# Performance work log

Measured on AMD Instinct MI355X. Metric: run time of the kernel, lower is better.

## Reference

```python
import jax, jax.numpy as jnp
import numpy as np

N_NODES = 32768
N_EDGES = 524288
NODE_DIM, POS_DIM, EDGE_DIM = 44, 8, 1
HID, OUT, LAYERS, HEADS = 128, 128, 3, 4
DK = HID // HEADS
LN_EPS = 1e-5


def _linear_w(key, fan_in, fan_out):
    return (jax.random.normal(key, (fan_in, fan_out), jnp.float32) / np.sqrt(fan_in)).astype(jnp.float32)


def _ln(x, g, b):
    m = jnp.mean(x, axis=-1, keepdims=True)
    v = jnp.var(x, axis=-1, keepdims=True)
    return (x - m) * jax.lax.rsqrt(v + LN_EPS) * g + b


def setup_inputs() -> dict:
    key = jax.random.key(0)
    ks = jax.random.split(key, 16)
    inp = {
        'feats': jax.random.normal(ks[0], (N_NODES, NODE_DIM), jnp.float32),
        'lap_pos_enc': jax.random.normal(ks[1], (N_NODES, POS_DIM), jnp.float32),
        'edge_feats': jax.random.normal(ks[2], (N_EDGES, EDGE_DIM), jnp.float32),
        'src': jax.random.randint(ks[3], (N_EDGES,), 0, N_NODES, jnp.int32),
        'dst': jax.random.randint(ks[4], (N_EDGES,), 0, N_NODES, jnp.int32),
        # input projections
        'W_node': _linear_w(ks[5], NODE_DIM, HID), 'b_node': jnp.zeros((HID,), jnp.float32),
        'W_pos': _linear_w(ks[6], POS_DIM, HID), 'b_pos': jnp.zeros((HID,), jnp.float32),
        'W_edge': _linear_w(ks[7], EDGE_DIM, HID), 'b_edge': jnp.zeros((HID,), jnp.float32),
    }
    # per-layer stacked params (all layers are HID->HID since OUT==HID)
    def stack(k, fi, fo):
        kk = jax.random.split(k, LAYERS)
        return jnp.stack([_linear_w(kk[i], fi, fo) for i in range(LAYERS)])
    inp['Wq'] = stack(ks[8], HID, HID)
    inp['Wk'] = stack(ks[9], HID, HID)
    inp['Wv'] = stack(ks[10], HID, HID)
    inp['We'] = stack(ks[11], HID, HID)
    inp['W_lin'] = stack(ks[12], HID, HID)
    inp['b_lin'] = jnp.zeros((LAYERS, HID), jnp.float32)
    inp['g1'] = jnp.ones((LAYERS, HID), jnp.float32)
    inp['be1'] = jnp.zeros((LAYERS, HID), jnp.float32)
    inp['Wf1'] = stack(ks[13], HID, 2 * HID)
    inp['bf1'] = jnp.zeros((LAYERS, 2 * HID), jnp.float32)
    inp['Wf2'] = stack(ks[14], 2 * HID, HID)
    inp['bf2'] = jnp.zeros((LAYERS, HID), jnp.float32)
    inp['g2'] = jnp.ones((LAYERS, HID), jnp.float32)
    inp['be2'] = jnp.zeros((LAYERS, HID), jnp.float32)
    return inp


def reference(feats, lap_pos_enc, edge_feats,
              W_node, b_node, W_pos, b_pos, W_edge, b_edge,
              Wq, Wk, Wv, We, W_lin, b_lin, g1, be1,
              Wf1, bf1, Wf2, bf2, g2, be2, src, dst):
    n = feats.shape[0]
    inv_sqrt_dk = np.float32(1.0 / np.sqrt(DK))
    h = feats @ W_node + b_node + lap_pos_enc @ W_pos + b_pos      # [N, HID]
    e = edge_feats @ W_edge + b_edge                               # [E, HID] (shared across layers)
    for i in range(LAYERS):
        Q = (h @ Wq[i]).reshape(n, HEADS, DK)
        K = (h @ Wk[i]).reshape(n, HEADS, DK)
        V = (h @ Wv[i]).reshape(n, HEADS, DK)
        E = (e @ We[i]).reshape(-1, HEADS, DK)                     # [E, H, DK]
        # raw score [E, H, 1] broadcast against (1+E) -> [E, H, DK] (faithful to source)
        score = jnp.sum(K[src] * Q[dst], axis=-1, keepdims=True) * inv_sqrt_dk
        score = score * (1.0 + E)
        alpha = jnp.exp(score)                                      # [E, H, DK]
        Z = jnp.maximum(jax.ops.segment_sum(alpha, dst, num_segments=n), 1e-6)
        h_out = jax.ops.segment_sum(V[src] * alpha, dst, num_segments=n) / Z
        h_out = h_out.reshape(n, HEADS * DK)
        h = h + h_out @ W_lin[i] + b_lin[i]                        # residual + dropout(identity)
        h = _ln(h, g1[i], be1[i])
        h2 = jax.nn.relu(h @ Wf1[i] + bf1[i]) @ Wf2[i] + bf2[i]
        h = _ln(h + h2, g2[i], be2[i])
    # dgl.mean_nodes over a single graph -> [1, OUT]; readout LayerNorm is never applied in source
    return jnp.mean(h, axis=0, keepdims=True)
```

## Files before the change

kernel.cpp:

```cpp
#include <hip/hip_runtime.h>
#include <hip/hip_bf16.h>

#define N_NODES 32768
#define N_EDGES 524288
#define LN_EPS 1e-5f

typedef unsigned short ushort_t;
typedef __attribute__((ext_vector_type(8))) short short8v;
typedef __attribute__((ext_vector_type(4))) float float4v;
typedef __attribute__((ext_vector_type(2))) float float2v;

__device__ __forceinline__ float bf2f(ushort_t u) {
    return __uint_as_float(((unsigned int)u) << 16);
}
__device__ __forceinline__ ushort_t f2bf(float f) {
    unsigned int u = __float_as_uint(f);
    unsigned int r = (u + 0x7FFFu + ((u >> 16) & 1u)) >> 16;
    return (ushort_t)r;
}
__device__ __forceinline__ float lo16(unsigned int x) { return __uint_as_float(x << 16); }
__device__ __forceinline__ float hi16(unsigned int x) { return __uint_as_float(x & 0xFFFF0000u); }

#if __has_builtin(__builtin_amdgcn_exp2f)
#define EXP2(x) __builtin_amdgcn_exp2f(x)
#else
#define EXP2(x) exp2f(x)
#endif

#define OFF_WNODE 0
#define OFF_BNODE 5632
#define OFF_WPOS  5760
#define OFF_BPOS  6784
#define OFF_WEDGE 6912
#define OFF_BEDGE 7040
#define OFF_BLIN  7168
#define OFF_G1    7552
#define OFF_BE1   7936
#define OFF_BF1   8320
#define OFF_BF2   9088
#define OFF_G2    9472
#define OFF_BE2   9856
#define CONV_TOTAL 10240

#define REC_QKV(i)  ((i) * 96)
#define REC_WLIN(i) (288 + (i) * 32)
#define REC_WF1(i)  (384 + (i) * 64)
#define REC_WF2(i)  (576 + (i) * 64)
#define REC_TOTAL   768

#define LDS_STRIDE 264
#define LDS_FSTRIDE 132

__global__ void detect_kernel(const unsigned int* __restrict__ wn, int* __restrict__ flag) {
    __shared__ int s[256];
    int t = threadIdx.x;
    int cnt = 0;
    for (int i = t; i < 2816; i += 256) {
        unsigned int b = (wn[i] >> 8) & 0x7F;
        cnt += (b >= 0x3A && b <= 0x40) ? 1 : 0;
    }
    s[t] = cnt;
    __syncthreads();
    for (int off = 128; off > 0; off >>= 1) {
        if (t < off) s[t] += s[t + off];
        __syncthreads();
    }
    if (t == 0) *flag = (s[0] > 1408) ? 1 : 0;
}

struct ConvArgs { const void* src[13]; };

__global__ void convert_kernel(ConvArgs a, const int* __restrict__ flag,
                               float* __restrict__ dst) {
    int gid = blockIdx.x * 256 + threadIdx.x;
    if (gid >= CONV_TOTAL) return;
    const int off[14] = {OFF_WNODE, OFF_BNODE, OFF_WPOS, OFF_BPOS, OFF_WEDGE, OFF_BEDGE,
                         OFF_BLIN, OFF_G1, OFF_BE1, OFF_BF1, OFF_BF2, OFF_G2, OFF_BE2,
                         CONV_TOTAL};
    int s = 0;
#pragma unroll
    for (int i = 1; i < 13; ++i) s += (gid >= off[i]) ? 1 : 0;
    int local = gid - off[s];
    if (*flag)
        dst[gid] = bf2f(((const ushort_t*)a.src[s])[local]);
    else
        dst[gid] = ((const float*)a.src[s])[local];
}

__global__ void swz_kernel(const void* __restrict__ Wq, const void* __restrict__ Wk,
                           const void* __restrict__ Wv, const void* __restrict__ Wlin,
                           const void* __restrict__ Wf1, const void* __restrict__ Wf2,
                           const void* __restrict__ We, const void* __restrict__ wedge,
                           const void* __restrict__ bedge,
                           const int* __restrict__ flag,
                           ushort_t* __restrict__ swz,
                           float* __restrict__ u, float* __restrict__ c1) {
    const bool isbf = (*flag != 0);
    if (blockIdx.x >= 192) {
        int l = blockIdx.x - 192;
        int d = threadIdx.x;
        if (d >= 128) return;
        float uu = 0.f, cc = 0.f;
        if (isbf) {
            const ushort_t* Wl = (const ushort_t*)We + (size_t)l * 16384;
            const ushort_t* we_ = (const ushort_t*)wedge;
            const ushort_t* be_ = (const ushort_t*)bedge;
#pragma unroll 4
            for (int k = 0; k < 128; ++k) {
                float w = bf2f(Wl[k * 128 + d]);
                uu = fmaf(bf2f(we_[k]), w, uu);
                cc = fmaf(bf2f(be_[k]), w, cc);
            }
        } else {
            const float* Wl = (const float*)We + (size_t)l * 16384;
            const float* we_ = (const float*)wedge;
            const float* be_ = (const float*)bedge;
#pragma unroll 4
            for (int k = 0; k < 128; ++k) {
                float w = Wl[k * 128 + d];
                uu = fmaf(we_[k], w, uu);
                cc = fmaf(be_[k], w, cc);
            }
        }
        const float scale = 0.17677669529663687f * 1.4426950408889634f;
        u[l * 128 + d] = uu * scale;
        c1[l * 128 + d] = (1.f + cc) * scale;
        return;
    }
    int gid = blockIdx.x * 256 + threadIdx.x;
    int lane = gid & 63;
    int rec = gid >> 6;
    int col = lane & 15, quad = lane >> 4;
    const void* src;
    size_t base;
    int ct, kb, OC;
    if (rec < 288) {
        int layer = rec / 96, r2 = rec % 96;
        ct = r2 >> 2; kb = r2 & 3;
        int seg = ct >> 3;
        src = (seg == 0) ? Wq : ((seg == 1) ? Wk : Wv);
        base = (size_t)layer * 16384; OC = 128; ct &= 7;
    } else if (rec < 384) {
        int r = rec - 288, layer = r / 32, r2 = r % 32;
        ct = r2 >> 2; kb = r2 & 3;
        src = Wlin; base = (size_t)layer * 16384; OC = 128;
    } else if (rec < 576) {
        int r = rec - 384, layer = r / 64, r2 = r % 64;
        ct = r2 >> 2; kb = r2 & 3;
        src = Wf1; base = (size_t)layer * 32768; OC = 256;
    } else {
        int r = rec - 576, layer = r / 64, r2 = r % 64;
        ct = r2 >> 3; kb = r2 & 7;
        src = Wf2; base = (size_t)layer * 32768; OC = 128;
    }
    int n = ct * 16 + col;
    ushort_t v[8];
    if (isbf) {
        const ushort_t* s16 = (const ushort_t*)src + base;
#pragma unroll
        for (int j = 0; j < 8; ++j) v[j] = s16[(size_t)(kb * 32 + quad * 8 + j) * OC + n];
    } else {
        const float* s32 = (const float*)src + base;
#pragma unroll
        for (int j = 0; j < 8; ++j) v[j] = f2bf(s32[(size_t)(kb * 32 + quad * 8 + j) * OC + n]);
    }
    ushort_t* o = swz + (size_t)rec * 512 + lane * 8;
#pragma unroll
    for (int j = 0; j < 8; ++j) o[j] = v[j];
}

__global__ void input_proj_kernel(const void* __restrict__ feats,
                                  const void* __restrict__ lap,
                                  const float* __restrict__ conv,
                                  const int* __restrict__ flag,
                                  const int* __restrict__ dstidx,
                                  int* __restrict__ deg,
                                  float* __restrict__ h, ushort_t* __restrict__ hb) {
    int gid = blockIdx.x * 256 + threadIdx.x;
    if (gid < N_EDGES) atomicAdd(&deg[dstidx[gid]], 1);
    int node = gid >> 5;
    int cg = (gid & 31) * 4;
    bool isbf = (*flag != 0);
    const float* Wn = conv + OFF_WNODE;
    const float* Wp = conv + OFF_WPOS;

    float4 b1 = *(const float4*)(conv + OFF_BNODE + cg);
    float4 b2 = *(const float4*)(conv + OFF_BPOS + cg);
    float a0 = b1.x + b2.x, a1 = b1.y + b2.y, a2 = b1.z + b2.z, a3 = b1.w + b2.w;

#define ACC(fv, Wbase, kk)                                            \
    {                                                                 \
        float4 wv_ = *(const float4*)(Wbase + (size_t)(kk) * 128 + cg); \
        a0 = fmaf(fv, wv_.x, a0);                                     \
        a1 = fmaf(fv, wv_.y, a1);                                     \
        a2 = fmaf(fv, wv_.z, a2);                                     \
        a3 = fmaf(fv, wv_.w, a3);                                     \
    }

    if (isbf) {
        const ushort_t* frow = (const ushort_t*)feats + (size_t)node * 44;
        const ushort_t* prow = (const ushort_t*)lap + (size_t)node * 8;
#pragma unroll
        for (int i = 0; i < 11; ++i) {
            ushort4 f = *(const ushort4*)(frow + i * 4);
            ACC(bf2f(f.x), Wn, i * 4 + 0)
            ACC(bf2f(f.y), Wn, i * 4 + 1)
            ACC(bf2f(f.z), Wn, i * 4 + 2)
            ACC(bf2f(f.w), Wn, i * 4 + 3)
        }
#pragma unroll
        for (int i = 0; i < 2; ++i) {
            ushort4 f = *(const ushort4*)(prow + i * 4);
            ACC(bf2f(f.x), Wp, i * 4 + 0)
            ACC(bf2f(f.y), Wp, i * 4 + 1)
            ACC(bf2f(f.z), Wp, i * 4 + 2)
            ACC(bf2f(f.w), Wp, i * 4 + 3)
        }
    } else {
        const float4* frow = (const float4*)((const float*)feats + (size_t)node * 44);
        const float4* prow = (const float4*)((const float*)lap + (size_t)node * 8);
#pragma unroll
        for (int i = 0; i < 11; ++i) {
            float4 f = frow[i];
            ACC(f.x, Wn, i * 4 + 0)
            ACC(f.y, Wn, i * 4 + 1)
            ACC(f.z, Wn, i * 4 + 2)
            ACC(f.w, Wn, i * 4 + 3)
        }
#pragma unroll
        for (int i = 0; i < 2; ++i) {
            float4 f = prow[i];
            ACC(f.x, Wp, i * 4 + 0)
            ACC(f.y, Wp, i * 4 + 1)
            ACC(f.z, Wp, i * 4 + 2)
            ACC(f.w, Wp, i * 4 + 3)
        }
    }
#undef ACC

    size_t idx = (size_t)node * 128 + cg;
    *(float4*)(h + idx) = make_float4(a0, a1, a2, a3);
    ushort4 ob;
    ob.x = f2bf(a0); ob.y = f2bf(a1); ob.z = f2bf(a2); ob.w = f2bf(a3);
    *(ushort4*)(hb + idx) = ob;
}

__global__ void scan_kernel(const int* __restrict__ deg, int* __restrict__ rowstart,
                            int* __restrict__ cursor) {
    __shared__ int lds[1024];
    int t = threadIdx.x;
    int base = t * 32;
    int v[32];
    int csum = 0;
#pragma unroll
    for (int j = 0; j < 8; ++j) {
        int4 x = *(const int4*)(deg + base + j * 4);
        v[j * 4 + 0] = x.x; v[j * 4 + 1] = x.y;
        v[j * 4 + 2] = x.z; v[j * 4 + 3] = x.w;
        csum += x.x + x.y + x.z + x.w;
    }
    lds[t] = csum;
    __syncthreads();
    for (int off = 1; off < 1024; off <<= 1) {
        int x = (t >= off) ? lds[t - off] : 0;
        __syncthreads();
        lds[t] += x;
        __syncthreads();
    }
    int excl = lds[t] - csum;
    int running = excl;
#pragma unroll
    for (int j = 0; j < 8; ++j) {
        int4 w;
        w.x = running; running += v[j * 4 + 0];
        w.y = running; running += v[j * 4 + 1];
        w.z = running; running += v[j * 4 + 2];
        w.w = running; running += v[j * 4 + 3];
        *(int4*)(rowstart + base + j * 4) = w;
        *(int4*)(cursor + base + j * 4) = w;
    }
    if (t == 1023) rowstart[N_NODES] = running;
}

__global__ void scatter_kernel(const int* __restrict__ src, const int* __restrict__ dst,
                               const void* __restrict__ ef, const int* __restrict__ flag,
                               int* __restrict__ cursor,
                               unsigned int* __restrict__ edges) {
    int e = blockIdx.x * 256 + threadIdx.x;
    if (e < N_EDGES) {
        ushort_t efb = (*flag != 0) ? ((const ushort_t*)ef)[e]
                                    : f2bf(((const float*)ef)[e]);
        int d = dst[e];
        int p = atomicAdd(&cursor[d], 1);
        edges[p] = (unsigned int)src[e] | ((unsigned int)efb << 16);
    }
}

template <int KB>
__global__ __launch_bounds__(256) void qkv_gemm(
    const ushort_t* __restrict__ A,
    const ushort_t* __restrict__ Bswz,
    ushort_t* __restrict__ outQ,
    unsigned char* __restrict__ outKV) {
    const int K = KB * 32;
    const int tid = threadIdx.x;
    const int wv = tid >> 6, lane = tid & 63;
    const int col = lane & 15, quad = lane >> 4;
    const int m0 = blockIdx.x * 64 + wv * 16;
    const int ct0 = blockIdx.y * 8;

    float4v acc[8];
#pragma unroll
    for (int ct = 0; ct < 8; ++ct) acc[ct] = (float4v){0.f, 0.f, 0.f, 0.f};

    const ushort_t* Ap = A + (size_t)(m0 + col) * K + quad * 8;
    const ushort_t* Bp = Bswz + (size_t)ct0 * KB * 512 + lane * 8;

#pragma unroll
    for (int kb = 0; kb < KB; ++kb) {
        short8v a = *(const short8v*)(Ap + kb * 32);
#pragma unroll
        for (int ct = 0; ct < 8; ++ct) {
            short8v b = *(const short8v*)(Bp + (size_t)(ct * KB + kb) * 512);
            acc[ct] = __builtin_amdgcn_mfma_f32_16x16x32_bf16(a, b, acc[ct], 0, 0, 0);
        }
    }

    const int rowb = m0 + quad * 4;
    const int seg = blockIdx.y;
    if (seg == 0) {
#pragma unroll
        for (int ct = 0; ct < 8; ++ct) {
            int j = ct * 16 + col;
#pragma unroll
            for (int r = 0; r < 4; ++r)
                outQ[(size_t)(rowb + r) * 128 + j] = f2bf(acc[ct][r]);
        }
    } else {
        const int vofs = (seg == 2) ? 8 : 0;
#pragma unroll
        for (int ct = 0; ct < 8; ++ct) {
            int j = ct * 16 + col;
            int off = ((j >> 3) * 16) + (j & 7) + vofs;
#pragma unroll
            for (int r = 0; r < 4; ++r) {
                float a = acc[ct][r];
                float b = __shfl_xor(a, 1, 64);
                if ((col & 1) == 0) {
                    unsigned short pk = (unsigned short)
                        __builtin_amdgcn_cvt_pk_fp8_f32(a, b, 0, false);
                    *(ushort_t*)(outKV + (size_t)(rowb + r) * 256 + off) = pk;
                }
            }
        }
    }
}

__global__ __launch_bounds__(64, 2) void ffn_kernel(
    const ushort_t* __restrict__ HOUT,
    const ushort_t* __restrict__ BWL,
    const ushort_t* __restrict__ BF1,
    const ushort_t* __restrict__ BF2,
    const ushort_t* __restrict__ BQKV,
    const float* __restrict__ bl,
    const float* __restrict__ g1v, const float* __restrict__ be1v,
    const float* __restrict__ bf1v,
    const float* __restrict__ bf2v,
    const float* __restrict__ g2v, const float* __restrict__ be2v,
    float* __restrict__ h,
    ushort_t* __restrict__ outQ,
    unsigned char* __restrict__ outKV,
    float* __restrict__ macc,
    const int fuse_qkv, const int do_mean) {
    __shared__ __align__(16) char ldsraw[16 * 528];
    ushort_t* ldsu = (ushort_t*)ldsraw;
    float* ldsf = (float*)ldsraw;
    const int lane = threadIdx.x & 63;
    const int col = lane & 15, quad = lane >> 4;
    const int m0 = blockIdx.x * 16;
    const int rowb = m0 + quad * 4;
    const int lrowc = quad * 4;
    const int lrowa = col;

    float4v acc[8];
#pragma unroll
    for (int ct = 0; ct < 8; ++ct) acc[ct] = (float4v){0.f, 0.f, 0.f, 0.f};
    const ushort_t* Ap = HOUT + (size_t)(m0 + col) * 128 + quad * 8;
#pragma unroll
    for (int kb = 0; kb < 4; ++kb) {
        short8v a = *(const short8v*)(Ap + kb * 32);
#pragma unroll
        for (int ct = 0; ct < 8; ++ct) {
            short8v b = *(const short8v*)(BWL + (size_t)(ct * 4 + kb) * 512 + lane * 8);
            acc[ct] = __builtin_amdgcn_mfma_f32_16x16x32_bf16(a, b, acc[ct], 0, 0, 0);
        }
    }

    float val[8][4], s[4] = {0.f, 0.f, 0.f, 0.f}, ss[4] = {0.f, 0.f, 0.f, 0.f};
#pragma unroll
    for (int ct = 0; ct < 8; ++ct) {
        float bi = bl[ct * 16 + col];
#pragma unroll
        for (int r = 0; r < 4; ++r) {
            float v = acc[ct][r] + bi + h[(size_t)(rowb + r) * 128 + ct * 16 + col];
            val[ct][r] = v;
            s[r] += v;
            ss[r] += v * v;
        }
    }
#pragma unroll
    for (int mask = 1; mask < 16; mask <<= 1) {
#pragma unroll
        for (int r = 0; r < 4; ++r) {
            s[r] += __shfl_xor(s[r], mask, 64);
            ss[r] += __shfl_xor(ss[r], mask, 64);
        }
    }
#pragma unroll
    for (int r = 0; r < 4; ++r) {
        float mean = s[r] * (1.f / 128.f);
        float var = ss[r] * (1.f / 128.f) - mean * mean;
        s[r] = mean;
        ss[r] = rsqrtf(var + LN_EPS);
    }
#pragma unroll
    for (int ct = 0; ct < 8; ++ct) {
        float gg = g1v[ct * 16 + col], bb = be1v[ct * 16 + col];
#pragma unroll
        for (int r = 0; r < 4; ++r) {
            float o = (val[ct][r] - s[r]) * ss[r] * gg + bb;
            val[ct][r] = o;
            ldsu[(lrowc + r) * LDS_STRIDE + ct * 16 + col] = f2bf(o);
        }
    }
    __syncthreads();

    short8v af[4];
#pragma unroll
    for (int kb = 0; kb < 4; ++kb)
        af[kb] = *(const short8v*)&ldsu[lrowa * LDS_STRIDE + kb * 32 + quad * 8];

    float4v acc2[16];
#pragma unroll
    for (int ct = 0; ct < 16; ++ct) acc2[ct] = (float4v){0.f, 0.f, 0.f, 0.f};
#pragma unroll
    for (int kb = 0; kb < 4; ++kb) {
#pragma unroll
        for (int ct = 0; ct < 16; ++ct) {
            short8v b = *(const short8v*)(BF1 + (size_t)(ct * 4 + kb) * 512 + lane * 8);
            acc2[ct] = __builtin_amdgcn_mfma_f32_16x16x32_bf16(af[kb], b, acc2[ct], 0, 0, 0);
        }
    }
    __syncthreads();

#pragma unroll
    for (int ct = 0; ct < 16; ++ct) {
        float bi = bf1v[ct * 16 + col];
#pragma unroll
        for (int r = 0; r < 4; ++r) {
            float v = fmaxf(acc2[ct][r] + bi, 0.f);
            ldsu[(lrowc + r) * LDS_STRIDE + ct * 16 + col] = f2bf(v);
        }
    }
    __syncthreads();

    float4v acc3[8];
#pragma unroll
    for (int ct = 0; ct < 8; ++ct) acc3[ct] = (float4v){0.f, 0.f, 0.f, 0.f};
#pragma unroll
    for (int kb = 0; kb < 8; ++kb) {
        short8v a = *(const short8v*)&ldsu[lrowa * LDS_STRIDE + kb * 32 + quad * 8];
#pragma unroll
        for (int ct = 0; ct < 8; ++ct) {
            short8v b = *(const short8v*)(BF2 + (size_t)(ct * 8 + kb) * 512 + lane * 8);
            acc3[ct] = __builtin_amdgcn_mfma_f32_16x16x32_bf16(a, b, acc3[ct], 0, 0, 0);
        }
    }

    float s2[4] = {0.f, 0.f, 0.f, 0.f}, ss2[4] = {0.f, 0.f, 0.f, 0.f};
#pragma unroll
    for (int ct = 0; ct < 8; ++ct) {
        float bi = bf2v[ct * 16 + col];
#pragma unroll
        for (int r = 0; r < 4; ++r) {
            float v = acc3[ct][r] + bi + val[ct][r];
            val[ct][r] = v;
            s2[r] += v;
            ss2[r] += v * v;
        }
    }
#pragma unroll
    for (int mask = 1; mask < 16; mask <<= 1) {
#pragma unroll
        for (int r = 0; r < 4; ++r) {
            s2[r] += __shfl_xor(s2[r], mask, 64);
            ss2[r] += __shfl_xor(ss2[r], mask, 64);
        }
    }
#pragma unroll
    for (int r = 0; r < 4; ++r) {
        float mean = s2[r] * (1.f / 128.f);
        float var = ss2[r] * (1.f / 128.f) - mean * mean;
        s2[r] = mean;
        ss2[r] = rsqrtf(var + LN_EPS);
    }
    __syncthreads();
#pragma unroll
    for (int ct = 0; ct < 8; ++ct) {
        float gg = g2v[ct * 16 + col], bb = be2v[ct * 16 + col];
#pragma unroll
        for (int r = 0; r < 4; ++r) {
            float o = (val[ct][r] - s2[r]) * ss2[r] * gg + bb;
            ldsf[(lrowc + r) * LDS_FSTRIDE + ct * 16 + col] = o;
        }
    }
    __syncthreads();

#pragma unroll
    for (int j = 0; j < 8; ++j) {
        int p = lane + j * 64;
        int row = p >> 5;
        int c4 = p & 31;
        float4 vv = *(const float4*)&ldsf[row * LDS_FSTRIDE + c4 * 4];
        *(float4*)&h[(size_t)(m0 + row) * 128 + c4 * 4] = vv;
    }

    if (fuse_qkv) {
        short8v afq[4];
#pragma unroll
        for (int kb = 0; kb < 4; ++kb) {
            float4 fa = *(const float4*)&ldsf[lrowa * LDS_FSTRIDE + kb * 32 + quad * 8];
            float4 fb = *(const float4*)&ldsf[lrowa * LDS_FSTRIDE + kb * 32 + quad * 8 + 4];
            short8v t;
            t[0] = (short)f2bf(fa.x); t[1] = (short)f2bf(fa.y);
            t[2] = (short)f2bf(fa.z); t[3] = (short)f2bf(fa.w);
            t[4] = (short)f2bf(fb.x); t[5] = (short)f2bf(fb.y);
            t[6] = (short)f2bf(fb.z); t[7] = (short)f2bf(fb.w);
            afq[kb] = t;
        }
#pragma unroll
        for (int seg = 0; seg < 3; ++seg) {
            float4v qacc[8];
#pragma unroll
            for (int ct = 0; ct < 8; ++ct) qacc[ct] = (float4v){0.f, 0.f, 0.f, 0.f};
#pragma unroll
            for (int kb = 0; kb < 4; ++kb) {
#pragma unroll
                for (int ct = 0; ct < 8; ++ct) {
                    short8v b = *(const short8v*)(BQKV +
                        (size_t)((seg * 8 + ct) * 4 + kb) * 512 + lane * 8);
                    qacc[ct] = __builtin_amdgcn_mfma_f32_16x16x32_bf16(afq[kb], b,
                                                                       qacc[ct], 0, 0, 0);
                }
            }
            if (seg == 0) {
#pragma unroll
                for (int ct = 0; ct < 8; ++ct) {
                    int j = ct * 16 + col;
#pragma unroll
                    for (int r = 0; r < 4; ++r)
                        outQ[(size_t)(rowb + r) * 128 + j] = f2bf(qacc[ct][r]);
                }
            } else {
                const int vofs = (seg == 2) ? 8 : 0;
#pragma unroll
                for (int ct = 0; ct < 8; ++ct) {
                    int j = ct * 16 + col;
                    int off = ((j >> 3) * 16) + (j & 7) + vofs;
#pragma unroll
                    for (int r = 0; r < 4; ++r) {
                        float a = qacc[ct][r];
                        float b = __shfl_xor(a, 1, 64);
                        if ((col & 1) == 0) {
                            unsigned short pk = (unsigned short)
                                __builtin_amdgcn_cvt_pk_fp8_f32(a, b, 0, false);
                            *(ushort_t*)(outKV + (size_t)(rowb + r) * 256 + off) = pk;
                        }
                    }
                }
            }
        }
    }

    if (do_mean) {
        int c0 = lane * 2;
        float sm0 = 0.f, sm1 = 0.f;
#pragma unroll
        for (int row = 0; row < 16; ++row) {
            sm0 += ldsf[row * LDS_FSTRIDE + c0];
            sm1 += ldsf[row * LDS_FSTRIDE + c0 + 1];
        }
        atomicAdd(&macc[c0], sm0);
        atomicAdd(&macc[c0 + 1], sm1);
    }
}

__global__ __launch_bounds__(64) void agg_kernel(
    const ushort_t* __restrict__ Q, const unsigned char* __restrict__ KV,
    const int* __restrict__ rowstart, const unsigned int* __restrict__ edges,
    const float* __restrict__ u, const float* __restrict__ c1,
    ushort_t* __restrict__ hout) {
    const int lane = threadIdx.x & 63;
    const int v = blockIdx.x;
    const int sub = lane & 15;
    const int grp = lane >> 4;

    uint4 qu = *(const uint4*)(Q + (size_t)v * 128 + sub * 8);
    float q0 = lo16(qu.x), q1 = hi16(qu.x), q2 = lo16(qu.y), q3 = hi16(qu.y);
    float q4 = lo16(qu.z), q5 = hi16(qu.z), q6 = lo16(qu.w), q7 = hi16(qu.w);
    float4 uva = *(const float4*)(u + sub * 8);
    float4 uvb = *(const float4*)(u + sub * 8 + 4);
    float4 cva = *(const float4*)(c1 + sub * 8);
    float4 cvb = *(const float4*)(c1 + sub * 8 + 4);

    float m = -1.0e38f;
    float sA[8] = {0.f, 0.f, 0.f, 0.f, 0.f, 0.f, 0.f, 0.f};
    float o[8] = {0.f, 0.f, 0.f, 0.f, 0.f, 0.f, 0.f, 0.f};

    const int start = rowstart[v];
    const int deg = rowstart[v + 1] - start;
    const int nfull = deg >> 2;
    const unsigned int* ep = edges + start + grp;

#define AGG_COMPUTE(PE, KVv, MASKED, VALID)                                      \
    {                                                                            \
        float ef_ = __uint_as_float((PE) & 0xFFFF0000u);                         \
        float2v k01 = __builtin_amdgcn_cvt_pk_f32_fp8((KVv).x, false);           \
        float2v k23 = __builtin_amdgcn_cvt_pk_f32_fp8((KVv).x, true);            \
        float2v k45 = __builtin_amdgcn_cvt_pk_f32_fp8((KVv).y, false);           \
        float2v k67 = __builtin_amdgcn_cvt_pk_f32_fp8((KVv).y, true);            \
        float p_ = k01[0] * q0;                                                  \
        p_ = fmaf(k01[1], q1, p_);                                               \
        p_ = fmaf(k23[0], q2, p_);                                               \
        p_ = fmaf(k23[1], q3, p_);                                               \
        p_ = fmaf(k45[0], q4, p_);                                               \
        p_ = fmaf(k45[1], q5, p_);                                               \
        p_ = fmaf(k67[0], q6, p_);                                               \
        p_ = fmaf(k67[1], q7, p_);                                               \
        p_ += __shfl_xor(p_, 1, 64);                                             \
        p_ += __shfl_xor(p_, 2, 64);                                             \
        float x0 = p_ * fmaf(ef_, uva.x, cva.x);                                 \
        float x1 = p_ * fmaf(ef_, uva.y, cva.y);                                 \
        float x2 = p_ * fmaf(ef_, uva.z, cva.z);                                 \
        float x3 = p_ * fmaf(ef_, uva.w, cva.w);                                 \
        float x4 = p_ * fmaf(ef_, uvb.x, cvb.x);                                 \
        float x5 = p_ * fmaf(ef_, uvb.y, cvb.y);                                 \
        float x6 = p_ * fmaf(ef_, uvb.z, cvb.z);                                 \
        float x7 = p_ * fmaf(ef_, uvb.w, cvb.w);                                 \
        if (MASKED) {                                                            \
            x0 = (VALID) ? x0 : -1.0e38f; x1 = (VALID) ? x1 : -1.0e38f;          \
            x2 = (VALID) ? x2 : -1.0e38f; x3 = (VALID) ? x3 : -1.0e38f;          \
            x4 = (VALID) ? x4 : -1.0e38f; x5 = (VALID) ? x5 : -1.0e38f;          \
            x6 = (VALID) ? x6 : -1.0e38f; x7 = (VALID) ? x7 : -1.0e38f;          \
        }                                                                        \
        float xm = fmaxf(fmaxf(fmaxf(x0, x1), fmaxf(x2, x3)),                    \
                         fmaxf(fmaxf(x4, x5), fmaxf(x6, x7)));                   \
        if (xm > m) {                                                            \
            float nm = xm + 6.0f;                                                \
            float sc = EXP2(m - nm);                                             \
            sA[0] *= sc; sA[1] *= sc; sA[2] *= sc; sA[3] *= sc;                  \
            sA[4] *= sc; sA[5] *= sc; sA[6] *= sc; sA[7] *= sc;                  \
            o[0] *= sc; o[1] *= sc; o[2] *= sc; o[3] *= sc;                      \
            o[4] *= sc; o[5] *= sc; o[6] *= sc; o[7] *= sc;                      \
            m = nm;                                                              \
        }                                                                        \
        float e0 = EXP2(x0 - m), e1 = EXP2(x1 - m);                              \
        float e2 = EXP2(x2 - m), e3 = EXP2(x3 - m);                              \
        float e4 = EXP2(x4 - m), e5 = EXP2(x5 - m);                              \
        float e6 = EXP2(x6 - m), e7 = EXP2(x7 - m);                              \
        sA[0] += e0; sA[1] += e1; sA[2] += e2; sA[3] += e3;                      \
        sA[4] += e4; sA[5] += e5; sA[6] += e6; sA[7] += e7;                      \
        float2v v01 = __builtin_amdgcn_cvt_pk_f32_fp8((KVv).z, false);           \
        float2v v23 = __builtin_amdgcn_cvt_pk_f32_fp8((KVv).z, true);            \
        float2v v45 = __builtin_amdgcn_cvt_pk_f32_fp8((KVv).w, false);           \
        float2v v67 = __builtin_amdgcn_cvt_pk_f32_fp8((KVv).w, true);            \
        o[0] = fmaf(v01[0], e0, o[0]);                                           \
        o[1] = fmaf(v01[1], e1, o[1]);                                           \
        o[2] = fmaf(v23[0], e2, o[2]);                                           \
        o[3] = fmaf(v23[1], e3, o[3]);                                           \
        o[4] = fmaf(v45[0], e4, o[4]);                                           \
        o[5] = fmaf(v45[1], e5, o[5]);                                           \
        o[6] = fmaf(v67[0], e6, o[6]);                                           \
        o[7] = fmaf(v67[1], e7, o[7]);                                           \
    }

    int it = 0;
    for (; it + 4 <= nfull; it += 4) {
        unsigned int pe0 = ep[4 * it];
        unsigned int pe1 = ep[4 * it + 4];
        unsigned int pe2 = ep[4 * it + 8];
        unsigned int pe3 = ep[4 * it + 12];
        uint4 kv0 = *(const uint4*)(KV + (size_t)(pe0 & 0xFFFFu) * 256 + sub * 16);
        uint4 kv1 = *(const uint4*)(KV + (size_t)(pe1 & 0xFFFFu) * 256 + sub * 16);
        uint4 kv2 = *(const uint4*)(KV + (size_t)(pe2 & 0xFFFFu) * 256 + sub * 16);
        uint4 kv3 = *(const uint4*)(KV + (size_t)(pe3 & 0xFFFFu) * 256 + sub * 16);
        AGG_COMPUTE(pe0, kv0, false, true)
        AGG_COMPUTE(pe1, kv1, false, true)
        AGG_COMPUTE(pe2, kv2, false, true)
        AGG_COMPUTE(pe3, kv3, false, true)
    }
    if (it + 2 <= nfull) {
        unsigned int pe0 = ep[4 * it];
        unsigned int pe1 = ep[4 * it + 4];
        uint4 kv0 = *(const uint4*)(KV + (size_t)(pe0 & 0xFFFFu) * 256 + sub * 16);
        uint4 kv1 = *(const uint4*)(KV + (size_t)(pe1 & 0xFFFFu) * 256 + sub * 16);
        AGG_COMPUTE(pe0, kv0, false, true)
        AGG_COMPUTE(pe1, kv1, false, true)
        it += 2;
    }
    if (it < nfull) {
        unsigned int pe0 = ep[4 * it];
        uint4 kv0 = *(const uint4*)(KV + (size_t)(pe0 & 0xFFFFu) * 256 + sub * 16);
        AGG_COMPUTE(pe0, kv0, false, true)
    }
    const int rem = deg & 3;
    if (rem) {
        bool valid = grp < rem;
        unsigned int pe = valid ? ep[4 * nfull] : edges[start];
        uint4 kv = *(const uint4*)(KV + (size_t)(pe & 0xFFFFu) * 256 + sub * 16);
        AGG_COMPUTE(pe, kv, true, valid)
    }
#undef AGG_COMPUTE

#pragma unroll
    for (int mask = 16; mask <= 32; mask <<= 1) {
        float mo = __shfl_xor(m, mask, 64);
        float mm = fmaxf(m, mo);
        float sca = EXP2(m - mm);
        float scb = EXP2(mo - mm);
#pragma unroll
        for (int j = 0; j < 8; ++j) {
            float t = __shfl_xor(sA[j], mask, 64);
            sA[j] = sA[j] * sca + t * scb;
            t = __shfl_xor(o[j], mask, 64);
            o[j] = o[j] * sca + t * scb;
        }
        m = mm;
    }

    if (grp == 0) {
        float zc = 1e-6f * EXP2(-m);
        uint4 ou;
        unsigned int w0, w1;
        float z;
        z = fmaxf(fmaxf(sA[0], zc), 1e-37f); w0 = f2bf(o[0] / z);
        z = fmaxf(fmaxf(sA[1], zc), 1e-37f); w1 = f2bf(o[1] / z);
        ou.x = w0 | (w1 << 16);
        z = fmaxf(fmaxf(sA[2], zc), 1e-37f); w0 = f2bf(o[2] / z);
        z = fmaxf(fmaxf(sA[3], zc), 1e-37f); w1 = f2bf(o[3] / z);
        ou.y = w0 | (w1 << 16);
        z = fmaxf(fmaxf(sA[4], zc), 1e-37f); w0 = f2bf(o[4] / z);
        z = fmaxf(fmaxf(sA[5], zc), 1e-37f); w1 = f2bf(o[5] / z);
        ou.z = w0 | (w1 << 16);
        z = fmaxf(fmaxf(sA[6], zc), 1e-37f); w0 = f2bf(o[6] / z);
        z = fmaxf(fmaxf(sA[7], zc), 1e-37f); w1 = f2bf(o[7] / z);
        ou.w = w0 | (w1 << 16);
        *(uint4*)(hout + (size_t)v * 128 + sub * 8) = ou;
    }
}

__global__ void finalize_kernel(const float* __restrict__ macc, void* __restrict__ out,
                                const int* __restrict__ flag) {
    int t = threadIdx.x;
    float v = macc[t] * (1.f / (float)N_NODES);
    if (*flag)
        ((ushort_t*)out)[t] = f2bf(v);
    else
        ((float*)out)[t] = v;
}

extern "C" void kernel_launch(void* const* d_in, const int* in_sizes, int n_in,
                              void* d_out, int out_size, void* d_ws, size_t ws_size,
                              hipStream_t stream) {
    const int* src = (const int*)d_in[3];
    const int* dst = (const int*)d_in[4];

    char* w = (char*)d_ws;
    const size_t MB = 1u << 20;
    float* h        = (float*)(w);
    ushort_t* hb    = (ushort_t*)(w + 16 * MB);
    ushort_t* Qh    = (ushort_t*)(w + 24 * MB);
    unsigned char* KVf8 = (unsigned char*)(w + 32 * MB);
    char* aux       = w + 48 * MB;
    int* deg        = (int*)(aux);
    int* rowstart   = (int*)(aux + 0x40000);
    int* cursor     = (int*)(aux + 0x80000);
    unsigned int* edges = (unsigned int*)(aux + 0xC0000);
    float* ubuf     = (float*)(aux + 0xC0000 + 2 * MB);
    float* cbuf     = ubuf + 3 * 128;
    float* macc     = cbuf + 3 * 128;
    int* flag       = (int*)(macc + 128);
    float* conv     = (float*)(aux + 0xC0000 + 2 * MB + 4096);
    ushort_t* swz   = (ushort_t*)((char*)conv + CONV_TOTAL * 4);

    hipMemsetAsync(deg, 0, N_NODES * sizeof(int), stream);
    hipMemsetAsync(macc, 0, 128 * sizeof(float), stream);

    detect_kernel<<<1, 256, 0, stream>>>((const unsigned int*)d_in[5], flag);

    ConvArgs ca;
    ca.src[0] = d_in[5];
    ca.src[1] = d_in[6];
    ca.src[2] = d_in[7];
    ca.src[3] = d_in[8];
    ca.src[4] = d_in[9];
    ca.src[5] = d_in[10];
    ca.src[6] = d_in[16];
    ca.src[7] = d_in[17];
    ca.src[8] = d_in[18];
    ca.src[9] = d_in[20];
    ca.src[10] = d_in[22];
    ca.src[11] = d_in[23];
    ca.src[12] = d_in[24];
    convert_kernel<<<(CONV_TOTAL + 255) / 256, 256, 0, stream>>>(ca, flag, conv);

    swz_kernel<<<192 + 3, 256, 0, stream>>>(
        d_in[11], d_in[12], d_in[13], d_in[15], d_in[19], d_in[21],
        d_in[14], d_in[9], d_in[10], flag, swz, ubuf, cbuf);

    input_proj_kernel<<<N_NODES * 32 / 256, 256, 0, stream>>>(d_in[0], d_in[1], conv,
                                                              flag, dst, deg, h, hb);
    scan_kernel<<<1, 1024, 0, stream>>>(deg, rowstart, cursor);
    scatter_kernel<<<N_EDGES / 256, 256, 0, stream>>>(src, dst, d_in[2], flag, cursor,
                                                      edges);

    qkv_gemm<4><<<dim3(N_NODES / 64, 3), 256, 0, stream>>>(
        hb, swz + (size_t)REC_QKV(0) * 512, Qh, KVf8);

    for (int i = 0; i < 3; ++i) {
        const ushort_t* swzWL  = swz + (size_t)REC_WLIN(i) * 512;
        const ushort_t* swzF1  = swz + (size_t)REC_WF1(i) * 512;
        const ushort_t* swzF2  = swz + (size_t)REC_WF2(i) * 512;
        const ushort_t* swzQn  = swz + (size_t)REC_QKV(i < 2 ? i + 1 : 0) * 512;

        agg_kernel<<<N_NODES, 64, 0, stream>>>(Qh, KVf8, rowstart, edges,
                                               ubuf + i * 128, cbuf + i * 128, hb);

        ffn_kernel<<<N_NODES / 16, 64, 0, stream>>>(
            hb, swzWL, swzF1, swzF2, swzQn,
            conv + OFF_BLIN + i * 128, conv + OFF_G1 + i * 128, conv + OFF_BE1 + i * 128,
            conv + OFF_BF1 + i * 256,
            conv + OFF_BF2 + i * 128, conv + OFF_G2 + i * 128, conv + OFF_BE2 + i * 128,
            h, Qh, KVf8, macc,
            (i < 2) ? 1 : 0, (i == 2) ? 1 : 0);
    }

    finalize_kernel<<<1, 128, 0, stream>>>(macc, d_out, flag);
}
```

Before: 524.2 us.

## Unfuse QKV projection from FFN kernel and run dedicated qkv_gemm per layer

```diff
diff --git a/kernel.cpp b/kernel.cpp
--- a/kernel.cpp
+++ b/kernel.cpp
@@ -356,22 +356,20 @@
     }
 }
 
+template <int DO_MEAN>
 __global__ __launch_bounds__(64, 2) void ffn_kernel(
     const ushort_t* __restrict__ HOUT,
     const ushort_t* __restrict__ BWL,
     const ushort_t* __restrict__ BF1,
     const ushort_t* __restrict__ BF2,
-    const ushort_t* __restrict__ BQKV,
     const float* __restrict__ bl,
     const float* __restrict__ g1v, const float* __restrict__ be1v,
     const float* __restrict__ bf1v,
     const float* __restrict__ bf2v,
     const float* __restrict__ g2v, const float* __restrict__ be2v,
     float* __restrict__ h,
-    ushort_t* __restrict__ outQ,
-    unsigned char* __restrict__ outKV,
-    float* __restrict__ macc,
-    const int fuse_qkv, const int do_mean) {
+    ushort_t* __restrict__ hb,
+    float* __restrict__ macc) {
     __shared__ __align__(16) char ldsraw[16 * 528];
     ushort_t* ldsu = (ushort_t*)ldsraw;
     float* ldsf = (float*)ldsraw;
@@ -524,65 +522,22 @@
         float4 vv = *(const float4*)&ldsf[row * LDS_FSTRIDE + c4 * 4];
         *(float4*)&h[(size_t)(m0 + row) * 128 + c4 * 4] = vv;
     }
-
-    if (fuse_qkv) {
-        short8v afq[4];
-#pragma unroll
-        for (int kb = 0; kb < 4; ++kb) {
-            float4 fa = *(const float4*)&ldsf[lrowa * LDS_FSTRIDE + kb * 32 + quad * 8];
-            float4 fb = *(const float4*)&ldsf[lrowa * LDS_FSTRIDE + kb * 32 + quad * 8 + 4];
-            short8v t;
-            t[0] = (short)f2bf(fa.x); t[1] = (short)f2bf(fa.y);
-            t[2] = (short)f2bf(fa.z); t[3] = (short)f2bf(fa.w);
-            t[4] = (short)f2bf(fb.x); t[5] = (short)f2bf(fb.y);
-            t[6] = (short)f2bf(fb.z); t[7] = (short)f2bf(fb.w);
-            afq[kb] = t;
-        }
-#pragma unroll
-        for (int seg = 0; seg < 3; ++seg) {
-            float4v qacc[8];
-#pragma unroll
-            for (int ct = 0; ct < 8; ++ct) qacc[ct] = (float4v){0.f, 0.f, 0.f, 0.f};
-#pragma unroll
-            for (int kb = 0; kb < 4; ++kb) {
-#pragma unroll
-                for (int ct = 0; ct < 8; ++ct) {
-                    short8v b = *(const short8v*)(BQKV +
-                        (size_t)((seg * 8 + ct) * 4 + kb) * 512 + lane * 8);
-                    qacc[ct] = __builtin_amdgcn_mfma_f32_16x16x32_bf16(afq[kb], b,
-                                                                       qacc[ct], 0, 0, 0);
-                }
-            }
-            if (seg == 0) {
-#pragma unroll
-                for (int ct = 0; ct < 8; ++ct) {
-                    int j = ct * 16 + col;
-#pragma unroll
-                    for (int r = 0; r < 4; ++r)
-                        outQ[(size_t)(rowb + r) * 128 + j] = f2bf(qacc[ct][r]);
-                }
-            } else {
-                const int vofs = (seg == 2) ? 8 : 0;
-#pragma unroll
-                for (int ct = 0; ct < 8; ++ct) {
-                    int j = ct * 16 + col;
-                    int off = ((j >> 3) * 16) + (j & 7) + vofs;
-#pragma unroll
-                    for (int r = 0; r < 4; ++r) {
-                        float a = qacc[ct][r];
-                        float b = __shfl_xor(a, 1, 64);
-                        if ((col & 1) == 0) {
-                            unsigned short pk = (unsigned short)
-                                __builtin_amdgcn_cvt_pk_fp8_f32(a, b, 0, false);
-                            *(ushort_t*)(outKV + (size_t)(rowb + r) * 256 + off) = pk;
-                        }
-                    }
-                }
-            }
-        }
-    }
-
-    if (do_mean) {
+#pragma unroll
+    for (int j = 0; j < 4; ++j) {
+        int p = lane + j * 64;
+        int row = p >> 4;
+        int c8 = p & 15;
+        float4 va = *(const float4*)&ldsf[row * LDS_FSTRIDE + c8 * 8];
+        float4 vb = *(const float4*)&ldsf[row * LDS_FSTRIDE + c8 * 8 + 4];
+        uint4 ou;
+        ou.x = (unsigned)f2bf(va.x) | ((unsigned)f2bf(va.y) << 16);
+        ou.y = (unsigned)f2bf(va.z) | ((unsigned)f2bf(va.w) << 16);
+        ou.z = (unsigned)f2bf(vb.x) | ((unsigned)f2bf(vb.y) << 16);
+        ou.w = (unsigned)f2bf(vb.z) | ((unsigned)f2bf(vb.w) << 16);
+        *(uint4*)&hb[(size_t)(m0 + row) * 128 + c8 * 8] = ou;
+    }
+
+    if (DO_MEAN) {
         int c0 = lane * 2;
         float sm0 = 0.f, sm1 = 0.f;
 #pragma unroll
@@ -824,25 +779,31 @@
     scatter_kernel<<<N_EDGES / 256, 256, 0, stream>>>(src, dst, d_in[2], flag, cursor,
                                                       edges);
 
-    qkv_gemm<4><<<dim3(N_NODES / 64, 3), 256, 0, stream>>>(
-        hb, swz + (size_t)REC_QKV(0) * 512, Qh, KVf8);
-
     for (int i = 0; i < 3; ++i) {
+        const ushort_t* swzQKV = swz + (size_t)REC_QKV(i) * 512;
         const ushort_t* swzWL  = swz + (size_t)REC_WLIN(i) * 512;
         const ushort_t* swzF1  = swz + (size_t)REC_WF1(i) * 512;
         const ushort_t* swzF2  = swz + (size_t)REC_WF2(i) * 512;
-        const ushort_t* swzQn  = swz + (size_t)REC_QKV(i < 2 ? i + 1 : 0) * 512;
+
+        qkv_gemm<4><<<dim3(N_NODES / 64, 3), 256, 0, stream>>>(hb, swzQKV, Qh, KVf8);
 
         agg_kernel<<<N_NODES, 64, 0, stream>>>(Qh, KVf8, rowstart, edges,
                                                ubuf + i * 128, cbuf + i * 128, hb);
 
-        ffn_kernel<<<N_NODES / 16, 64, 0, stream>>>(
-            hb, swzWL, swzF1, swzF2, swzQn,
-            conv + OFF_BLIN + i * 128, conv + OFF_G1 + i * 128, conv + OFF_BE1 + i * 128,
-            conv + OFF_BF1 + i * 256,
-            conv + OFF_BF2 + i * 128, conv + OFF_G2 + i * 128, conv + OFF_BE2 + i * 128,
-            h, Qh, KVf8, macc,
-            (i < 2) ? 1 : 0, (i == 2) ? 1 : 0);
+        if (i < 2)
+            ffn_kernel<0><<<N_NODES / 16, 64, 0, stream>>>(
+                hb, swzWL, swzF1, swzF2,
+                conv + OFF_BLIN + i * 128, conv + OFF_G1 + i * 128, conv + OFF_BE1 + i * 128,
+                conv + OFF_BF1 + i * 256,
+                conv + OFF_BF2 + i * 128, conv + OFF_G2 + i * 128, conv + OFF_BE2 + i * 128,
+                h, hb, macc);
+        else
+            ffn_kernel<1><<<N_NODES / 16, 64, 0, stream>>>(
+                hb, swzWL, swzF1, swzF2,
+                conv + OFF_BLIN + i * 128, conv + OFF_G1 + i * 128, conv + OFF_BE1 + i * 128,
+                conv + OFF_BF1 + i * 256,
+                conv + OFF_BF2 + i * 128, conv + OFF_G2 + i * 128, conv + OFF_BE2 + i * 128,
+                h, hb, macc);
     }
 
     finalize_kernel<<<1, 128, 0, stream>>>(macc, d_out, flag);
```

Result: slower. 565.0 us (+7.8%).
